# Kernel optimization log

Hardware: AMD Instinct MI355X
Metric: run time of the kernel (lower is better)

The kernel has to match this reference:

```python
import jax, jax.numpy as jnp
import numpy as np

EMB = 1024
HEADS = 16
HEADSIZE = EMB // HEADS


def _layernorm(x, gamma, beta, eps=1e-5):
    # LayerNorm over the last dim (headsize), affine.
    mu = jnp.mean(x, axis=-1, keepdims=True)
    var = jnp.var(x, axis=-1, keepdims=True)
    return (x - mu) * jax.lax.rsqrt(var + eps) * gamma + beta


def setup_inputs() -> dict:
    key = jax.random.key(0)
    ks = jax.random.split(key, 12)
    B, TI, TC = 4, 1024, 1024
    s = 1.0 / np.sqrt(EMB)
    inp = {
        "x": jax.random.normal(ks[0], (B, TI, EMB), dtype=jnp.float32),
        "context": jax.random.normal(ks[1], (B, TC, EMB), dtype=jnp.float32),
        # torch nn.Linear weights are (out, in); y = x @ W.T
        "Wq": jax.random.uniform(ks[2], (EMB, EMB), jnp.float32, -s, s),
        "Wk": jax.random.uniform(ks[3], (EMB, EMB), jnp.float32, -s, s),
        "Wv": jax.random.uniform(ks[4], (EMB, EMB), jnp.float32, -s, s),
        "Wu": jax.random.uniform(ks[5], (EMB, EMB), jnp.float32, -s, s),
        "bu": jax.random.uniform(ks[6], (EMB,), jnp.float32, -s, s),
        "q_gamma": jnp.ones((HEADSIZE,), jnp.float32),
        "q_beta": jnp.zeros((HEADSIZE,), jnp.float32),
        "k_gamma": jnp.ones((HEADSIZE,), jnp.float32),
        "k_beta": jnp.zeros((HEADSIZE,), jnp.float32),
    }
    return inp


def reference(x, context, Wq, Wk, Wv, Wu, bu, q_gamma, q_beta, k_gamma, k_beta):
    B, TI, E = x.shape
    TC = context.shape[1]
    T = TI + TC
    xc = jnp.concatenate([x, context], axis=1)  # [B, T, E]

    q = (x @ Wq.T).reshape(B, TI, HEADS, HEADSIZE)
    k = (xc @ Wk.T).reshape(B, T, HEADS, HEADSIZE)
    v = (xc @ Wv.T).reshape(B, T, HEADS, HEADSIZE)

    # optional QK-LayerNorm over headsize
    q = _layernorm(q, q_gamma, q_beta)
    k = _layernorm(k, k_gamma, k_beta)

    scale = E ** 0.25
    q = q / scale
    k = k / scale

    # scores: [B, H, TI, T]
    dot = jnp.einsum("bihd,bjhd->bhij", q, k)
    attn = jax.nn.softmax(dot, axis=-1)
    out = jnp.einsum("bhij,bjhd->bihd", attn, v).reshape(B, TI, E)
    return out @ Wu.T + bu
```

## Files before the change

kernel.cpp:

```cpp
#include <hip/hip_runtime.h>
#include <cstdint>


typedef unsigned short u16;
typedef __attribute__((ext_vector_type(8))) short bf16x8;
typedef __attribute__((ext_vector_type(4))) float f32x4;
typedef __attribute__((ext_vector_type(16))) float f32x16;
typedef __attribute__((ext_vector_type(4))) unsigned short u16x4;
typedef __attribute__((ext_vector_type(2))) unsigned int u32x2;

#define GLDS(gsrc, ldst)                                                              \
  __builtin_amdgcn_global_load_lds(                                                   \
      (const __attribute__((address_space(1))) unsigned int*)(gsrc),                  \
      (__attribute__((address_space(3))) unsigned int*)(ldst), 16, 0, 0)

__device__ __forceinline__ u16 f2bf(float x) {
  unsigned int u = __float_as_uint(x);
  u += 0x7fffu + ((u >> 16) & 1u);
  return (u16)(u >> 16);
}

__device__ __forceinline__ unsigned cvt_pk_bf16(float lo, float hi) {
  unsigned r;
  asm("v_cvt_pk_bf16_f32 %0, %1, %2" : "=v"(r) : "v"(lo), "v"(hi));
  return r;
}

__device__ __forceinline__ f32x4 mfma16(bf16x8 a, bf16x8 b, f32x4 c) {
  return __builtin_amdgcn_mfma_f32_16x16x32_bf16(a, b, c, 0, 0, 0);
}
__device__ __forceinline__ f32x16 mfma32(bf16x8 a, bf16x8 b, f32x16 c) {
  return __builtin_amdgcn_mfma_f32_32x32x16_bf16(a, b, c, 0, 0, 0);
}


__global__ __launch_bounds__(256) void cast_concat(const float* __restrict__ x,
                                                   const float* __restrict__ c,
                                                   u16* __restrict__ o) {
  const int n4 = (8 << 20) / 4;
  for (int i = blockIdx.x * blockDim.x + threadIdx.x; i < n4; i += gridDim.x * blockDim.x) {
    int elem = i * 4;
    int b = elem >> 21;
    int rem = elem & ((1 << 21) - 1);
    int r = rem >> 10;
    int e = rem & 1023;
    const float* src = (r < 1024) ? (x + ((((size_t)(b << 10)) + r) << 10) + e)
                                  : (c + ((((size_t)(b << 10)) + (r - 1024)) << 10) + e);
    float4 v = *(const float4*)src;
    u16x4 ov;
    ov.x = f2bf(v.x); ov.y = f2bf(v.y); ov.z = f2bf(v.z); ov.w = f2bf(v.w);
    *(u16x4*)(o + elem) = ov;
  }
}

__global__ __launch_bounds__(256) void cast_w(const float* __restrict__ w0,
                                              const float* __restrict__ w1,
                                              const float* __restrict__ w2,
                                              const float* __restrict__ w3,
                                              u16* __restrict__ o) {
  const int n4 = (4 << 20) / 4;
  for (int i = blockIdx.x * blockDim.x + threadIdx.x; i < n4; i += gridDim.x * blockDim.x) {
    int elem = i * 4;
    int sel = elem >> 20;
    int loc = elem & ((1 << 20) - 1);
    const float* s = (sel == 0) ? w0 : (sel == 1) ? w1 : (sel == 2) ? w2 : w3;
    float4 v = *(const float4*)(s + loc);
    u16x4 ov;
    ov.x = f2bf(v.x); ov.y = f2bf(v.y); ov.z = f2bf(v.z); ov.w = f2bf(v.w);
    *(u16x4*)(o + elem) = ov;
  }
}


__global__ __launch_bounds__(256)
void gemm_qkv(const u16* __restrict__ XCB, const u16* __restrict__ Wall,
              u16* __restrict__ QBB, u16* __restrict__ KBB, u16* __restrict__ VT,
              const float* __restrict__ qg, const float* __restrict__ qb,
              const float* __restrict__ kg, const float* __restrict__ kb,
              float sQ, float sK) {
  const int ny = blockIdx.y;
  const int which = ny >> 3;
  const int m0 = blockIdx.x << 7;
  if (which == 0 && (m0 & 2047) >= 1024) return;
  const int n0 = (ny & 7) << 7;
  const u16* Bw = Wall + ((size_t)which << 20);
  const int K = 1024, N = 1024;

  __shared__ alignas(16) u16 lA[2][128 * 32];
  __shared__ alignas(16) u16 lB[2][128 * 32];
  const int tid = threadIdx.x;
  const int wv = tid >> 6, l = tid & 63, g = l >> 4, c16 = l & 15;
  const int wr = wv >> 1, wc = wv & 1;

  f32x4 acc[4][4];
  const f32x4 z4 = {0.f, 0.f, 0.f, 0.f};
#pragma unroll
  for (int i = 0; i < 4; ++i)
#pragma unroll
    for (int j = 0; j < 4; ++j) acc[i][j] = z4;

  const int srow = tid >> 2;
  const int scA = (tid & 3) ^ ((srow >> 1) & 3);
  const u16* aSrc = XCB + (size_t)(m0 + srow) * K + scA * 8;
  const u16* bSrc = Bw + (size_t)(n0 + srow) * K + scA * 8;
  char* ldA = (char*)lA;
  char* ldB = (char*)lB;
  const int lof = wv * 1024;

#define STAGE_G(bi, kof)                                   \
  {                                                        \
    char* dA = ldA + (bi)*8192 + lof;                      \
    char* dB = ldB + (bi)*8192 + lof;                      \
    GLDS(aSrc + (kof), dA);                                \
    GLDS(aSrc + (size_t)64 * K + (kof), dA + 4096);        \
    GLDS(bSrc + (kof), dB);                                \
    GLDS(bSrc + (size_t)64 * K + (kof), dB + 4096);        \
  }

  STAGE_G(0, 0);
  __syncthreads();
  int buf = 0;
  for (int kt = 0; kt < 32; ++kt) {
    if (kt + 1 < 32) STAGE_G(buf ^ 1, (kt + 1) << 5);
    const char* bA = ldA + buf * 8192;
    const char* bB = ldB + buf * 8192;
    bf16x8 af[4], bfr[4];
#pragma unroll
    for (int mi = 0; mi < 4; ++mi) {
      int row = wr * 64 + mi * 16 + c16;
      af[mi] = *(const bf16x8*)(bA + row * 64 + ((g * 16) ^ (((row >> 1) & 3) << 4)));
    }
#pragma unroll
    for (int ni = 0; ni < 4; ++ni) {
      int row = wc * 64 + ni * 16 + c16;
      bfr[ni] = *(const bf16x8*)(bB + row * 64 + ((g * 16) ^ (((row >> 1) & 3) << 4)));
    }
    __builtin_amdgcn_s_setprio(1);
#pragma unroll
    for (int mi = 0; mi < 4; ++mi)
#pragma unroll
      for (int ni = 0; ni < 4; ++ni)
        acc[mi][ni] = mfma16(af[mi], bfr[ni], acc[mi][ni]);
    __builtin_amdgcn_s_setprio(0);
    __syncthreads();
    buf ^= 1;
  }
#undef STAGE_G

  if (which == 2) {
#pragma unroll
    for (int ni = 0; ni < 4; ++ni) {
      int col = n0 + wc * 64 + ni * 16 + c16;
      int hh = col >> 6, dd = col & 63;
#pragma unroll
      for (int mi = 0; mi < 4; ++mi) {
        int m = m0 + wr * 64 + mi * 16 + g * 4;
        int bb = m >> 11, tt = m & 2047;
        u16x4 o;
#pragma unroll
        for (int r = 0; r < 4; ++r) o[r] = f2bf(acc[mi][ni][r]);
        *(u16x4*)(VT + ((size_t)((bb * 16 + hh) * 64 + dd)) * 2048 + tt) = o;
      }
    }
  } else {
    const float* G = which ? kg : qg;
    const float* Bt = which ? kb : qb;
    const float osc = which ? sK : sQ;
    u16* Ob = which ? KBB : QBB;
#pragma unroll
    for (int mi = 0; mi < 4; ++mi) {
      float sum[4], sq[4];
#pragma unroll
      for (int r = 0; r < 4; ++r) {
        float s = 0.f, q = 0.f;
#pragma unroll
        for (int ni = 0; ni < 4; ++ni) {
          float v = acc[mi][ni][r];
          s += v;
          q += v * v;
        }
#pragma unroll
        for (int msk = 1; msk < 16; msk <<= 1) {
          s += __shfl_xor(s, msk);
          q += __shfl_xor(q, msk);
        }
        sum[r] = s;
        sq[r] = q;
      }
#pragma unroll
      for (int ni = 0; ni < 4; ++ni) {
        int dloc = ni * 16 + c16;
        int colg = n0 + wc * 64 + ni * 16 + c16;
        float gv = G[dloc], bv = Bt[dloc];
#pragma unroll
        for (int r = 0; r < 4; ++r) {
          float mean = sum[r] * (1.f / 64.f);
          float var = sq[r] * (1.f / 64.f) - mean * mean;
          float y = (acc[mi][ni][r] - mean) * rsqrtf(var + 1e-5f) * gv + bv;
          int row = m0 + wr * 64 + mi * 16 + g * 4 + r;
          int orow = which ? row : (((row >> 11) << 10) | (row & 1023));
          Ob[(size_t)orow * N + colg] = f2bf(y * osc);
        }
      }
    }
  }
}


__global__ __launch_bounds__(256)
void gemm_u64(const u16* __restrict__ A, const u16* __restrict__ Bw,
              float* __restrict__ Of, const float* __restrict__ bias) {
  const int K = 1024, N = 1024;
  __shared__ alignas(16) u16 lA[2][64 * 32];
  __shared__ alignas(16) u16 lB[2][128 * 32];
  const int tid = threadIdx.x;
  const int wv = tid >> 6, l = tid & 63, g = l >> 4, c16 = l & 15;
  const int wr = wv >> 1, wc = wv & 1;
  const int m0 = blockIdx.x << 6, n0 = blockIdx.y << 7;

  f32x4 acc[2][4];
  const f32x4 z4 = {0.f, 0.f, 0.f, 0.f};
#pragma unroll
  for (int i = 0; i < 2; ++i)
#pragma unroll
    for (int j = 0; j < 4; ++j) acc[i][j] = z4;

  const int srow = tid >> 2;
  const int sc = (tid & 3) ^ ((srow >> 1) & 3);
  const u16* aSrc = A + (size_t)(m0 + srow) * K + sc * 8;
  const u16* bSrc = Bw + (size_t)(n0 + srow) * K + sc * 8;
  char* ldA = (char*)lA;
  char* ldB = (char*)lB;
  const int lof = wv * 1024;

#define STAGE_U(bi, kof)                                   \
  {                                                        \
    char* dA = ldA + (bi)*4096 + lof;                      \
    char* dB = ldB + (bi)*8192 + lof;                      \
    GLDS(aSrc + (kof), dA);                                \
    GLDS(bSrc + (kof), dB);                                \
    GLDS(bSrc + (size_t)64 * K + (kof), dB + 4096);        \
  }

  STAGE_U(0, 0);
  __syncthreads();
  int buf = 0;
  for (int kt = 0; kt < 32; ++kt) {
    if (kt + 1 < 32) STAGE_U(buf ^ 1, (kt + 1) << 5);
    const char* bA = ldA + buf * 4096;
    const char* bB = ldB + buf * 8192;
    bf16x8 af[2], bfr[4];
#pragma unroll
    for (int mi = 0; mi < 2; ++mi) {
      int row = wr * 32 + mi * 16 + c16;
      af[mi] = *(const bf16x8*)(bA + row * 64 + ((g * 16) ^ (((row >> 1) & 3) << 4)));
    }
#pragma unroll
    for (int ni = 0; ni < 4; ++ni) {
      int row = wc * 64 + ni * 16 + c16;
      bfr[ni] = *(const bf16x8*)(bB + row * 64 + ((g * 16) ^ (((row >> 1) & 3) << 4)));
    }
    __builtin_amdgcn_s_setprio(1);
#pragma unroll
    for (int mi = 0; mi < 2; ++mi)
#pragma unroll
      for (int ni = 0; ni < 4; ++ni)
        acc[mi][ni] = mfma16(af[mi], bfr[ni], acc[mi][ni]);
    __builtin_amdgcn_s_setprio(0);
    __syncthreads();
    buf ^= 1;
  }
#undef STAGE_U

#pragma unroll
  for (int ni = 0; ni < 4; ++ni) {
    int col = n0 + wc * 64 + ni * 16 + c16;
    float bv = bias[col];
#pragma unroll
    for (int mi = 0; mi < 2; ++mi) {
      int row = m0 + wr * 32 + mi * 16 + g * 4;
      float* dst = Of + (size_t)row * N + col;
#pragma unroll
      for (int r = 0; r < 4; ++r) dst[(size_t)r * N] = acc[mi][ni][r] + bv;
    }
  }
}


__global__ __launch_bounds__(512, 4)
void attn_kernel(const u16* __restrict__ Q, const u16* __restrict__ Kb,
                 const u16* __restrict__ Vt, u16* __restrict__ AO) {
  __shared__ union alignas(16) {
    struct { u16 K[2][2][4096]; u16 V[2][2][4096]; } kv;
    float cmb[4][64][34];
  } sm;
  const int tid = threadIdx.x;
  const int wv = tid >> 6, l = tid & 63;
  const int w4 = wv & 3, kvh2 = wv >> 2;
  const int lq = l & 31, hi = l >> 5;
  const int h = blockIdx.x, b = blockIdx.y, qt = blockIdx.z;
  const int qrow = (b << 10) + (qt << 7) + (w4 << 5) + lq;

  const u16* qp = Q + (size_t)qrow * 1024 + h * 64 + hi * 8;
  bf16x8 qf[4];
#pragma unroll
  for (int kk = 0; kk < 4; ++kk) qf[kk] = *(const bf16x8*)(qp + 16 * kk);

  f32x16 acc[2];
#pragma unroll
  for (int d0 = 0; d0 < 2; ++d0)
#pragma unroll
    for (int i = 0; i < 16; ++i) acc[d0][i] = 0.f;
  float m_run = -1e30f, l_run = 0.f;

  const u16* Ksrc = Kb + ((size_t)(b * 2048) + l) * 1024 + h * 64 + w4 * 8;
  const u16* Vsrc = Vt + ((size_t)((b * 16 + h) * 64) + l) * 2048 + w4 * 8;

#define STAGE_KV(bi, it)                                    \
  {                                                         \
    const int kv0 = ((it) << 7) + (kvh2 << 6);              \
    char* dK = (char*)sm.kv.K[kvh2][bi] + w4 * 1024;        \
    char* dV = (char*)sm.kv.V[kvh2][bi] + w4 * 1024;        \
    const u16* ks = Ksrc + (size_t)kv0 * 1024;              \
    const u16* vs = Vsrc + kv0;                             \
    GLDS(ks, dK);                                           \
    GLDS(ks + 32, dK + 4096);                               \
    GLDS(vs, dV);                                           \
    GLDS(vs + 32, dV + 4096);                               \
  }

  STAGE_KV(0, 0);
  __syncthreads();
  int buf = 0;

  for (int it = 0; it < 16; ++it) {
    if (it + 1 < 16) STAGE_KV(buf ^ 1, it + 1);
    const char* bK = (const char*)sm.kv.K[kvh2][buf];
    const char* bV = (const char*)sm.kv.V[kvh2][buf];

    f32x16 s[2];
#pragma unroll
    for (int kvh = 0; kvh < 2; ++kvh)
#pragma unroll
      for (int i = 0; i < 16; ++i) s[kvh][i] = 0.f;
    __builtin_amdgcn_s_setprio(1);
#pragma unroll
    for (int kk = 0; kk < 4; ++kk) {
      const char* kbase = bK + (2 * kk + hi) * 1024;
      bf16x8 kf0 = *(const bf16x8*)(kbase + lq * 16);
      bf16x8 kf1 = *(const bf16x8*)(kbase + (32 + lq) * 16);
      s[0] = mfma32(kf0, qf[kk], s[0]);
      s[1] = mfma32(kf1, qf[kk], s[1]);
    }
    __builtin_amdgcn_s_setprio(0);

    float tm0 = fmaxf(s[0][0], s[1][0]), tm1 = fmaxf(s[0][1], s[1][1]);
    float tm2 = fmaxf(s[0][2], s[1][2]), tm3 = fmaxf(s[0][3], s[1][3]);
#pragma unroll
    for (int i = 4; i < 16; i += 4) {
      tm0 = fmaxf(tm0, fmaxf(s[0][i], s[1][i]));
      tm1 = fmaxf(tm1, fmaxf(s[0][i + 1], s[1][i + 1]));
      tm2 = fmaxf(tm2, fmaxf(s[0][i + 2], s[1][i + 2]));
      tm3 = fmaxf(tm3, fmaxf(s[0][i + 3], s[1][i + 3]));
    }
    float tm = fmaxf(fmaxf(tm0, tm1), fmaxf(tm2, tm3));
    tm = fmaxf(tm, __shfl_xor(tm, 32));
    if (!__all(tm <= m_run + 8.f)) {
      float mnew = fmaxf(m_run, tm);
      float corr = __builtin_amdgcn_exp2f(m_run - mnew);
      l_run *= corr;
#pragma unroll
      for (int d0 = 0; d0 < 2; ++d0)
#pragma unroll
        for (int i = 0; i < 16; ++i) acc[d0][i] *= corr;
      m_run = mnew;
    }
    float ts0 = 0.f, ts1 = 0.f, ts2 = 0.f, ts3 = 0.f;
#pragma unroll
    for (int kvh = 0; kvh < 2; ++kvh)
#pragma unroll
      for (int i = 0; i < 16; i += 4) {
        float p0 = __builtin_amdgcn_exp2f(s[kvh][i] - m_run);
        float p1 = __builtin_amdgcn_exp2f(s[kvh][i + 1] - m_run);
        float p2 = __builtin_amdgcn_exp2f(s[kvh][i + 2] - m_run);
        float p3 = __builtin_amdgcn_exp2f(s[kvh][i + 3] - m_run);
        s[kvh][i] = p0; s[kvh][i + 1] = p1; s[kvh][i + 2] = p2; s[kvh][i + 3] = p3;
        ts0 += p0; ts1 += p1; ts2 += p2; ts3 += p3;
      }
    float ts = (ts0 + ts1) + (ts2 + ts3);
    ts += __shfl_xor(ts, 32);
    l_run += ts;

    unsigned int pk[2][4][2];
#pragma unroll
    for (int kvh = 0; kvh < 2; ++kvh)
#pragma unroll
      for (int kp = 0; kp < 4; ++kp)
#pragma unroll
        for (int tt = 0; tt < 2; ++tt)
          pk[kvh][kp][tt] = cvt_pk_bf16(s[kvh][4 * kp + 2 * tt], s[kvh][4 * kp + 2 * tt + 1]);

    __builtin_amdgcn_s_setprio(1);
#pragma unroll
    for (int kk = 0; kk < 4; ++kk) {
      const int kvh = kk >> 1, kb = kk & 1;
      union { unsigned w[4]; bf16x8 v; } bw;
#pragma unroll
      for (int tt = 0; tt < 2; ++tt) {
        unsigned A0 = pk[kvh][2 * kb][tt];
        unsigned A1 = pk[kvh][2 * kb + 1][tt];
        unsigned S = (unsigned)__shfl_xor((int)(hi ? A0 : A1), 32);
        bw.w[tt] = hi ? S : A0;
        bw.w[2 + tt] = hi ? A1 : S;
      }
      const char* vbase = bV + (2 * kk + hi) * 1024;
      bf16x8 vf0 = *(const bf16x8*)(vbase + lq * 16);
      bf16x8 vf1 = *(const bf16x8*)(vbase + (32 + lq) * 16);
      acc[0] = mfma32(vf0, bw.v, acc[0]);
      acc[1] = mfma32(vf1, bw.v, acc[1]);
    }
    __builtin_amdgcn_s_setprio(0);
    __syncthreads();
    buf ^= 1;
  }
#undef STAGE_KV

  if (wv >= 4) {
    float* cp = sm.cmb[w4][l];
#pragma unroll
    for (int d0 = 0; d0 < 2; ++d0)
#pragma unroll
      for (int i = 0; i < 16; ++i) cp[d0 * 16 + i] = acc[d0][i];
    cp[32] = m_run;
    cp[33] = l_run;
  }
  __syncthreads();
  if (wv < 4) {
    const float* cp = sm.cmb[w4][l];
    float m1 = cp[32], l1 = cp[33];
    float mm = fmaxf(m_run, m1);
    float c0 = __builtin_amdgcn_exp2f(m_run - mm);
    float c1 = __builtin_amdgcn_exp2f(m1 - mm);
    float invl = 1.f / (l_run * c0 + l1 * c1);
    float s0 = c0 * invl, s1 = c1 * invl;
#pragma unroll
    for (int d0 = 0; d0 < 2; ++d0)
#pragma unroll
      for (int rg = 0; rg < 4; ++rg) {
        float v0 = acc[d0][4 * rg + 0] * s0 + cp[d0 * 16 + 4 * rg + 0] * s1;
        float v1 = acc[d0][4 * rg + 1] * s0 + cp[d0 * 16 + 4 * rg + 1] * s1;
        float v2 = acc[d0][4 * rg + 2] * s0 + cp[d0 * 16 + 4 * rg + 2] * s1;
        float v3 = acc[d0][4 * rg + 3] * s0 + cp[d0 * 16 + 4 * rg + 3] * s1;
        u32x2 o;
        o.x = cvt_pk_bf16(v0, v1);
        o.y = cvt_pk_bf16(v2, v3);
        int d = 32 * d0 + 8 * rg + 4 * hi;
        *(u32x2*)(AO + (size_t)qrow * 1024 + h * 64 + d) = o;
      }
  }
}


extern "C" void kernel_launch(void* const* d_in, const int* in_sizes, int n_in,
                              void* d_out, int out_size, void* d_ws, size_t ws_size,
                              hipStream_t stream) {
  const float* x = (const float*)d_in[0];
  const float* ctx = (const float*)d_in[1];
  const float* Wq = (const float*)d_in[2];
  const float* Wk = (const float*)d_in[3];
  const float* Wv = (const float*)d_in[4];
  const float* Wu = (const float*)d_in[5];
  const float* bu = (const float*)d_in[6];
  const float* qg = (const float*)d_in[7];
  const float* qb = (const float*)d_in[8];
  const float* kg = (const float*)d_in[9];
  const float* kb = (const float*)d_in[10];
  float* out = (float*)d_out;

  char* w = (char*)d_ws;
  u16* XCB = (u16*)(w);
  u16* WQB = (u16*)(w + ((size_t)16 << 20));
  u16* QBB = (u16*)(w + ((size_t)24 << 20));
  u16* KBB = (u16*)(w + ((size_t)32 << 20));
  u16* VT = (u16*)(w + ((size_t)48 << 20));
  u16* AO = (u16*)(w + ((size_t)64 << 20));

  const float invs = 0.17677669529663687f;
  const float invs_l2e = invs * 1.44269504088896f;

  cast_concat<<<2048, 256, 0, stream>>>(x, ctx, XCB);
  cast_w<<<1024, 256, 0, stream>>>(Wq, Wk, Wv, Wu, WQB);

  gemm_qkv<<<dim3(64, 24), 256, 0, stream>>>(XCB, WQB, QBB, KBB, VT,
                                             qg, qb, kg, kb, invs_l2e, invs);

  attn_kernel<<<dim3(16, 4, 8), 512, 0, stream>>>(QBB, KBB, VT, AO);

  gemm_u64<<<dim3(64, 8), 256, 0, stream>>>(AO, WQB + ((size_t)3 << 20), out, bu);
}
```

Before: 265.0 us.

## Triple-buffer LDS staging in QKV and output GEMMs with vmcnt-based waits

Both GEMM kernels move from double to triple LDS buffering. Loads are issued two k-tiles ahead, and each iteration waits only for the oldest group with s_waitcnt vmcnt before one barrier, instead of two full __syncthreads per iteration. The goal is to hide more global-load latency and cut barrier overhead. It raises LDS use, which can lower occupancy, and correctness relies on the manual vmcnt counts matching the number of loads issued per stage.

```diff
diff --git a/kernel.cpp b/kernel.cpp
--- a/kernel.cpp
+++ b/kernel.cpp
@@ -86,8 +86,8 @@
   const u16* Bw = Wall + ((size_t)which << 20);
   const int K = 1024, N = 1024;
 
-  __shared__ alignas(16) u16 lA[2][128 * 32];
-  __shared__ alignas(16) u16 lB[2][128 * 32];
+  __shared__ alignas(16) u16 lA[3][128 * 32];
+  __shared__ alignas(16) u16 lB[3][128 * 32];
   const int tid = threadIdx.x;
   const int wv = tid >> 6, l = tid & 63, g = l >> 4, c16 = l & 15;
   const int wr = wv >> 1, wc = wv & 1;
@@ -118,12 +118,18 @@
   }
 
   STAGE_G(0, 0);
-  __syncthreads();
-  int buf = 0;
+  STAGE_G(1, 32);
+  int cb = 0, sb = 2;
   for (int kt = 0; kt < 32; ++kt) {
-    if (kt + 1 < 32) STAGE_G(buf ^ 1, (kt + 1) << 5);
-    const char* bA = ldA + buf * 8192;
-    const char* bB = ldB + buf * 8192;
+    if (kt < 31) {
+      asm volatile("s_waitcnt vmcnt(4)" ::: "memory");
+    } else {
+      asm volatile("s_waitcnt vmcnt(0)" ::: "memory");
+    }
+    __builtin_amdgcn_s_barrier();
+    if (kt + 2 < 32) STAGE_G(sb, (kt + 2) << 5);
+    const char* bA = ldA + cb * 8192;
+    const char* bB = ldB + cb * 8192;
     bf16x8 af[4], bfr[4];
 #pragma unroll
     for (int mi = 0; mi < 4; ++mi) {
@@ -142,8 +148,8 @@
       for (int ni = 0; ni < 4; ++ni)
         acc[mi][ni] = mfma16(af[mi], bfr[ni], acc[mi][ni]);
     __builtin_amdgcn_s_setprio(0);
-    __syncthreads();
-    buf ^= 1;
+    cb = cb == 2 ? 0 : cb + 1;
+    sb = sb == 2 ? 0 : sb + 1;
   }
 #undef STAGE_G
 
@@ -211,8 +217,8 @@
 void gemm_u64(const u16* __restrict__ A, const u16* __restrict__ Bw,
               float* __restrict__ Of, const float* __restrict__ bias) {
   const int K = 1024, N = 1024;
-  __shared__ alignas(16) u16 lA[2][64 * 32];
-  __shared__ alignas(16) u16 lB[2][128 * 32];
+  __shared__ alignas(16) u16 lA[3][64 * 32];
+  __shared__ alignas(16) u16 lB[3][128 * 32];
   const int tid = threadIdx.x;
   const int wv = tid >> 6, l = tid & 63, g = l >> 4, c16 = l & 15;
   const int wr = wv >> 1, wc = wv & 1;
@@ -243,12 +249,18 @@
   }
 
   STAGE_U(0, 0);
-  __syncthreads();
-  int buf = 0;
+  STAGE_U(1, 32);
+  int cb = 0, sb = 2;
   for (int kt = 0; kt < 32; ++kt) {
-    if (kt + 1 < 32) STAGE_U(buf ^ 1, (kt + 1) << 5);
-    const char* bA = ldA + buf * 4096;
-    const char* bB = ldB + buf * 8192;
+    if (kt < 31) {
+      asm volatile("s_waitcnt vmcnt(3)" ::: "memory");
+    } else {
+      asm volatile("s_waitcnt vmcnt(0)" ::: "memory");
+    }
+    __builtin_amdgcn_s_barrier();
+    if (kt + 2 < 32) STAGE_U(sb, (kt + 2) << 5);
+    const char* bA = ldA + cb * 4096;
+    const char* bB = ldB + cb * 8192;
     bf16x8 af[2], bfr[4];
 #pragma unroll
     for (int mi = 0; mi < 2; ++mi) {
@@ -267,8 +279,8 @@
       for (int ni = 0; ni < 4; ++ni)
         acc[mi][ni] = mfma16(af[mi], bfr[ni], acc[mi][ni]);
     __builtin_amdgcn_s_setprio(0);
-    __syncthreads();
-    buf ^= 1;
+    cb = cb == 2 ? 0 : cb + 1;
+    sb = sb == 2 ? 0 : sb + 1;
   }
 #undef STAGE_U
 
```

After: 261.0 us. No clear change (-1.5%).

## Double K-tile depth to 64 in QKV and output GEMMs with 8-chunk swizzle

Applied to the files above, without the earlier changes.

Both GEMM kernels now stage 64-wide K slices per iteration instead of 32, halving the number of main-loop iterations and __syncthreads barriers. The shared-memory layout is changed to 128-byte rows with an XOR swizzle over 8 chunks so the wider rows stay bank-conflict free. Each stage issues more async global-to-LDS loads, and each kernel uses twice the LDS, which can lower occupancy.

```diff
diff --git a/kernel.cpp b/kernel.cpp
--- a/kernel.cpp
+++ b/kernel.cpp
@@ -86,8 +86,8 @@
   const u16* Bw = Wall + ((size_t)which << 20);
   const int K = 1024, N = 1024;
 
-  __shared__ alignas(16) u16 lA[2][128 * 32];
-  __shared__ alignas(16) u16 lB[2][128 * 32];
+  __shared__ alignas(16) u16 lA[2][128 * 64];
+  __shared__ alignas(16) u16 lB[2][128 * 64];
   const int tid = threadIdx.x;
   const int wv = tid >> 6, l = tid & 63, g = l >> 4, c16 = l & 15;
   const int wr = wv >> 1, wc = wv & 1;
@@ -99,49 +99,53 @@
 #pragma unroll
     for (int j = 0; j < 4; ++j) acc[i][j] = z4;
 
-  const int srow = tid >> 2;
-  const int scA = (tid & 3) ^ ((srow >> 1) & 3);
-  const u16* aSrc = XCB + (size_t)(m0 + srow) * K + scA * 8;
-  const u16* bSrc = Bw + (size_t)(n0 + srow) * K + scA * 8;
-  char* ldA = (char*)lA;
-  char* ldB = (char*)lB;
-  const int lof = wv * 1024;
+  const int srow = (wv << 3) + (l >> 3);
+  const int schk = (l & 7) ^ ((l >> 3) & 7);
+  const u16* aSrc = XCB + (size_t)(m0 + srow) * K + schk * 8;
+  const u16* bSrc = Bw + (size_t)(n0 + srow) * K + schk * 8;
 
 #define STAGE_G(bi, kof)                                   \
   {                                                        \
-    char* dA = ldA + (bi)*8192 + lof;                      \
-    char* dB = ldB + (bi)*8192 + lof;                      \
+    char* dA = (char*)lA + (bi)*16384 + wv * 1024;         \
+    char* dB = (char*)lB + (bi)*16384 + wv * 1024;         \
     GLDS(aSrc + (kof), dA);                                \
-    GLDS(aSrc + (size_t)64 * K + (kof), dA + 4096);        \
+    GLDS(aSrc + (size_t)32 * K + (kof), dA + 4096);        \
+    GLDS(aSrc + (size_t)64 * K + (kof), dA + 8192);        \
+    GLDS(aSrc + (size_t)96 * K + (kof), dA + 12288);       \
     GLDS(bSrc + (kof), dB);                                \
-    GLDS(bSrc + (size_t)64 * K + (kof), dB + 4096);        \
+    GLDS(bSrc + (size_t)32 * K + (kof), dB + 4096);        \
+    GLDS(bSrc + (size_t)64 * K + (kof), dB + 8192);        \
+    GLDS(bSrc + (size_t)96 * K + (kof), dB + 12288);       \
   }
 
   STAGE_G(0, 0);
   __syncthreads();
   int buf = 0;
-  for (int kt = 0; kt < 32; ++kt) {
-    if (kt + 1 < 32) STAGE_G(buf ^ 1, (kt + 1) << 5);
-    const char* bA = ldA + buf * 8192;
-    const char* bB = ldB + buf * 8192;
-    bf16x8 af[4], bfr[4];
-#pragma unroll
-    for (int mi = 0; mi < 4; ++mi) {
-      int row = wr * 64 + mi * 16 + c16;
-      af[mi] = *(const bf16x8*)(bA + row * 64 + ((g * 16) ^ (((row >> 1) & 3) << 4)));
-    }
-#pragma unroll
-    for (int ni = 0; ni < 4; ++ni) {
-      int row = wc * 64 + ni * 16 + c16;
-      bfr[ni] = *(const bf16x8*)(bB + row * 64 + ((g * 16) ^ (((row >> 1) & 3) << 4)));
-    }
-    __builtin_amdgcn_s_setprio(1);
-#pragma unroll
-    for (int mi = 0; mi < 4; ++mi)
-#pragma unroll
-      for (int ni = 0; ni < 4; ++ni)
-        acc[mi][ni] = mfma16(af[mi], bfr[ni], acc[mi][ni]);
-    __builtin_amdgcn_s_setprio(0);
+  for (int kt = 0; kt < 16; ++kt) {
+    if (kt + 1 < 16) STAGE_G(buf ^ 1, (kt + 1) << 6);
+    const char* bA = (const char*)lA + buf * 16384;
+    const char* bB = (const char*)lB + buf * 16384;
+#pragma unroll
+    for (int kk = 0; kk < 2; ++kk) {
+      bf16x8 af[4], bfr[4];
+#pragma unroll
+      for (int mi = 0; mi < 4; ++mi) {
+        int row = wr * 64 + mi * 16 + c16;
+        af[mi] = *(const bf16x8*)(bA + row * 128 + ((((kk << 2) + g) ^ (row & 7)) << 4));
+      }
+#pragma unroll
+      for (int ni = 0; ni < 4; ++ni) {
+        int row = wc * 64 + ni * 16 + c16;
+        bfr[ni] = *(const bf16x8*)(bB + row * 128 + ((((kk << 2) + g) ^ (row & 7)) << 4));
+      }
+      __builtin_amdgcn_s_setprio(1);
+#pragma unroll
+      for (int mi = 0; mi < 4; ++mi)
+#pragma unroll
+        for (int ni = 0; ni < 4; ++ni)
+          acc[mi][ni] = mfma16(af[mi], bfr[ni], acc[mi][ni]);
+      __builtin_amdgcn_s_setprio(0);
+    }
     __syncthreads();
     buf ^= 1;
   }
@@ -211,8 +215,8 @@
 void gemm_u64(const u16* __restrict__ A, const u16* __restrict__ Bw,
               float* __restrict__ Of, const float* __restrict__ bias) {
   const int K = 1024, N = 1024;
-  __shared__ alignas(16) u16 lA[2][64 * 32];
-  __shared__ alignas(16) u16 lB[2][128 * 32];
+  __shared__ alignas(16) u16 lA[2][64 * 64];
+  __shared__ alignas(16) u16 lB[2][128 * 64];
   const int tid = threadIdx.x;
   const int wv = tid >> 6, l = tid & 63, g = l >> 4, c16 = l & 15;
   const int wr = wv >> 1, wc = wv & 1;
@@ -225,48 +229,51 @@
 #pragma unroll
     for (int j = 0; j < 4; ++j) acc[i][j] = z4;
 
-  const int srow = tid >> 2;
-  const int sc = (tid & 3) ^ ((srow >> 1) & 3);
-  const u16* aSrc = A + (size_t)(m0 + srow) * K + sc * 8;
-  const u16* bSrc = Bw + (size_t)(n0 + srow) * K + sc * 8;
-  char* ldA = (char*)lA;
-  char* ldB = (char*)lB;
-  const int lof = wv * 1024;
+  const int srow = (wv << 3) + (l >> 3);
+  const int schk = (l & 7) ^ ((l >> 3) & 7);
+  const u16* aSrc = A + (size_t)(m0 + srow) * K + schk * 8;
+  const u16* bSrc = Bw + (size_t)(n0 + srow) * K + schk * 8;
 
 #define STAGE_U(bi, kof)                                   \
   {                                                        \
-    char* dA = ldA + (bi)*4096 + lof;                      \
-    char* dB = ldB + (bi)*8192 + lof;                      \
+    char* dA = (char*)lA + (bi)*8192 + wv * 1024;          \
+    char* dB = (char*)lB + (bi)*16384 + wv * 1024;         \
     GLDS(aSrc + (kof), dA);                                \
+    GLDS(aSrc + (size_t)32 * K + (kof), dA + 4096);        \
     GLDS(bSrc + (kof), dB);                                \
-    GLDS(bSrc + (size_t)64 * K + (kof), dB + 4096);        \
+    GLDS(bSrc + (size_t)32 * K + (kof), dB + 4096);        \
+    GLDS(bSrc + (size_t)64 * K + (kof), dB + 8192);        \
+    GLDS(bSrc + (size_t)96 * K + (kof), dB + 12288);       \
   }
 
   STAGE_U(0, 0);
   __syncthreads();
   int buf = 0;
-  for (int kt = 0; kt < 32; ++kt) {
-    if (kt + 1 < 32) STAGE_U(buf ^ 1, (kt + 1) << 5);
-    const char* bA = ldA + buf * 4096;
-    const char* bB = ldB + buf * 8192;
-    bf16x8 af[2], bfr[4];
-#pragma unroll
-    for (int mi = 0; mi < 2; ++mi) {
-      int row = wr * 32 + mi * 16 + c16;
-      af[mi] = *(const bf16x8*)(bA + row * 64 + ((g * 16) ^ (((row >> 1) & 3) << 4)));
-    }
-#pragma unroll
-    for (int ni = 0; ni < 4; ++ni) {
-      int row = wc * 64 + ni * 16 + c16;
-      bfr[ni] = *(const bf16x8*)(bB + row * 64 + ((g * 16) ^ (((row >> 1) & 3) << 4)));
-    }
-    __builtin_amdgcn_s_setprio(1);
-#pragma unroll
-    for (int mi = 0; mi < 2; ++mi)
-#pragma unroll
-      for (int ni = 0; ni < 4; ++ni)
-        acc[mi][ni] = mfma16(af[mi], bfr[ni], acc[mi][ni]);
-    __builtin_amdgcn_s_setprio(0);
+  for (int kt = 0; kt < 16; ++kt) {
+    if (kt + 1 < 16) STAGE_U(buf ^ 1, (kt + 1) << 6);
+    const char* bA = (const char*)lA + buf * 8192;
+    const char* bB = (const char*)lB + buf * 16384;
+#pragma unroll
+    for (int kk = 0; kk < 2; ++kk) {
+      bf16x8 af[2], bfr[4];
+#pragma unroll
+      for (int mi = 0; mi < 2; ++mi) {
+        int row = wr * 32 + mi * 16 + c16;
+        af[mi] = *(const bf16x8*)(bA + row * 128 + ((((kk << 2) + g) ^ (row & 7)) << 4));
+      }
+#pragma unroll
+      for (int ni = 0; ni < 4; ++ni) {
+        int row = wc * 64 + ni * 16 + c16;
+        bfr[ni] = *(const bf16x8*)(bB + row * 128 + ((((kk << 2) + g) ^ (row & 7)) << 4));
+      }
+      __builtin_amdgcn_s_setprio(1);
+#pragma unroll
+      for (int mi = 0; mi < 2; ++mi)
+#pragma unroll
+        for (int ni = 0; ni < 4; ++ni)
+          acc[mi][ni] = mfma16(af[mi], bfr[ni], acc[mi][ni]);
+      __builtin_amdgcn_s_setprio(0);
+    }
     __syncthreads();
     buf ^= 1;
   }
```

Measured after the change: 244.0 us. -7.9%, faster.
